# Kernel optimization log

Measured on AMD Instinct MI355X. Metric: run time of the kernel, lower is better.

Reference implementation:

```python
import jax, jax.numpy as jnp
import numpy as np

BN_EPS = 1e-5


def conv1x1(x, w, b):
    # x: [B,C,H,W], w: [O,C], b: [O]
    return jnp.einsum('bchw,oc->bohw', x, w) + b[None, :, None, None]


def dwconv3(x, w, b):
    # depthwise 3x3, SAME padding; w: [C,1,3,3]
    y = jax.lax.conv_general_dilated(
        x, w, window_strides=(1, 1), padding='SAME',
        feature_group_count=x.shape[1],
        dimension_numbers=('NCHW', 'OIHW', 'NCHW'))
    return y + b[None, :, None, None]


def setup_inputs() -> dict:
    key = jax.random.key(0)
    B, C, H, W, E = 8, 256, 80, 80, 2
    ks = jax.random.split(key, 16)

    def n(k, shape, sc=0.02):
        return jax.random.normal(k, shape, dtype=jnp.float32) * sc

    return {
        'x': jax.random.normal(ks[0], (B, C, H, W), dtype=jnp.float32),
        # BatchNorm2d (inference: running stats + affine)
        'bn_gamma': jnp.ones((C,), jnp.float32),
        'bn_beta': jnp.zeros((C,), jnp.float32),
        'bn_mean': n(ks[1], (C,), 0.1),
        'bn_var': jnp.abs(n(ks[2], (C,), 0.5)) + 1.0,
        # SpectralGating complex per-channel gate
        'alpha_real': n(ks[3], (1, C, 1, 1), 0.1),
        'alpha_imag': n(ks[4], (1, C, 1, 1), 0.1),
        # LocalMamba2D (fallback path)
        'pi_w': n(ks[5], (C, C)), 'pi_b': jnp.zeros((C,), jnp.float32),
        'dw_w': n(ks[6], (C, 1, 3, 3)), 'dw_b': jnp.zeros((C,), jnp.float32),
        'fpw_w': n(ks[7], (C, C)), 'fpw_b': jnp.zeros((C,), jnp.float32),
        'ffn1_w': n(ks[8], (C * E, C)), 'ffn1_b': jnp.zeros((C * E,), jnp.float32),
        'ffn2_w': n(ks[9], (C, C * E)), 'ffn2_b': jnp.zeros((C,), jnp.float32),
        'po_w': n(ks[10], (C, C)), 'po_b': jnp.zeros((C,), jnp.float32),
        # post 1x1 conv
        'post_w': n(ks[11], (C, C)), 'post_b': jnp.zeros((C,), jnp.float32),
    }


def reference(x, bn_gamma, bn_beta, bn_mean, bn_var, alpha_real, alpha_imag,
              pi_w, pi_b, dw_w, dw_b, fpw_w, fpw_b,
              ffn1_w, ffn1_b, ffn2_w, ffn2_b, po_w, po_b,
              post_w, post_b):
    res = x
    # pre_norm: BatchNorm2d in inference mode
    inv = jax.lax.rsqrt(bn_var + BN_EPS)
    h = (x - bn_mean[None, :, None, None]) * (bn_gamma * inv)[None, :, None, None] \
        + bn_beta[None, :, None, None]
    # SpectralGating: rfft2 (ortho) -> complex per-channel gate -> irfft2
    H, W = h.shape[2], h.shape[3]
    X = jnp.fft.rfft2(h, norm='ortho')              # [B,C,H,W//2+1] complex
    Y = X * (alpha_real + 1j * alpha_imag)
    h = jnp.fft.irfft2(Y, s=(H, W), norm='ortho')
    # LocalMamba2D fallback: proj_in -> dw3x3 -> GELU -> 1x1 -> FFN -> proj_out (+res)
    # H,W are multiples of window=8, so pad branch is a no-op.
    res2 = h
    t = conv1x1(h, pi_w, pi_b)
    y = jax.nn.gelu(dwconv3(t, dw_w, dw_b), approximate=False)
    y = conv1x1(y, fpw_w, fpw_b)
    y = jax.nn.gelu(conv1x1(y, ffn1_w, ffn1_b), approximate=False)
    y = conv1x1(y, ffn2_w, ffn2_b)
    h = conv1x1(y, po_w, po_b) + res2
    # post 1x1 conv + outer residual
    out = conv1x1(h, post_w, post_b)
    return out + res
```

## Files before the change

### kernel.cpp

```cpp
#include <hip/hip_runtime.h>
#include <cmath>

#define BB 8
#define CC 256
#define HH 80
#define WW 80
#define HWSZ 6400
#define PLANE_FLOATS (CC * HWSZ)
#define TENSOR_FLOATS (BB * PLANE_FLOATS)

using short8v = __attribute__((ext_vector_type(8))) short;
using f32x4  = __attribute__((ext_vector_type(4))) float;

__device__ __forceinline__ float gelu_exact(float v) {
    return 0.5f * v * (1.0f + erff(v * 0.70710678118654752440f));
}

__device__ __forceinline__ unsigned short f2bf(float f) {
    unsigned int u = __float_as_uint(f);
    unsigned int r = (u + 0x7FFFu + ((u >> 16) & 1u)) >> 16;
    return (unsigned short)r;
}
__device__ __forceinline__ float bf2f(unsigned short h) {
    return __uint_as_float(((unsigned int)h) << 16);
}

__global__ __launch_bounds__(256)
void combine_po_post(const float* __restrict__ po_w, const float* __restrict__ po_b,
                     const float* __restrict__ post_w, const float* __restrict__ post_b,
                     float* __restrict__ Wcomb, float* __restrict__ bcomb)
{
    __shared__ float red[256];
    const int o = blockIdx.x;
    const int c = threadIdx.x;
    const float* prow = post_w + (size_t)o * 256;
    float s = 0.f;
#pragma unroll 4
    for (int m = 0; m < 256; ++m)
        s = fmaf(prow[m], po_w[(size_t)m * 256 + c], s);
    Wcomb[(size_t)o * 512 + c] = s;
    Wcomb[(size_t)o * 512 + 256 + c] = prow[c];
    red[c] = prow[c] * po_b[c];
    __syncthreads();
    for (int st = 128; st > 0; st >>= 1) {
        if (c < st) red[c] += red[c + st];
        __syncthreads();
    }
    if (c == 0) bcomb[o] = red[0] + post_b[o];
}

struct PreAll {
    const float* src[7];
    int stride[7];
    int runs[7];
    int dstOff[7];
};

__global__ __launch_bounds__(256)
void preconvert_kernel(PreAll d, unsigned short* __restrict__ packH,
                       unsigned short* __restrict__ packL)
{
    const int m = blockIdx.y;
    const int r = blockIdx.x * 256 + threadIdx.x;
    if (r >= d.runs[m]) return;
    const int ks = r >> 10;
    const int rem = r & 1023;
    const int fi = rem >> 6;
    const int l = rem & 63;
    const int o = fi * 16 + (l & 15);
    const int c0 = ks * 32 + ((l >> 4)) * 8;
    const float* src = d.src[m] + (size_t)o * d.stride[m] + c0;
    short8v hv, lv;
#pragma unroll
    for (int j = 0; j < 8; ++j) {
        const float v = src[j];
        const unsigned short h = f2bf(v);
        const unsigned short lo = f2bf(v - bf2f(h));
        hv[j] = (short)h; lv[j] = (short)lo;
    }
    *(short8v*)(packH + d.dstOff[m] + (size_t)r * 8) = hv;
    *(short8v*)(packL + d.dstOff[m] + (size_t)r * 8) = lv;
}

struct GTab { float g[40]; };

__global__ __launch_bounds__(256)
void bn_gate_kernel(const float* __restrict__ x,
                    const float* __restrict__ gamma, const float* __restrict__ beta,
                    const float* __restrict__ mean,  const float* __restrict__ var,
                    const float* __restrict__ ar,    const float* __restrict__ ai,
                    float* __restrict__ out, GTab gt)
{
    __shared__ float sv[HWSZ];
    const int blk = blockIdx.x;
    const int c = blk & (CC - 1);
    const float sc = gamma[c] * rsqrtf(var[c] + 1e-5f);
    const float sh = beta[c] - mean[c] * sc;
    const float a = ar[c], bgate = ai[c];
    const size_t base = (size_t)blk * HWSZ;

    const float4* x4 = (const float4*)(x + base);
    float4* s4 = (float4*)sv;
    for (int i = threadIdx.x; i < HWSZ / 4; i += 256) {
        float4 v = x4[i];
        v.x = fmaf(sc, v.x, sh); v.y = fmaf(sc, v.y, sh);
        v.z = fmaf(sc, v.z, sh); v.w = fmaf(sc, v.w, sh);
        s4[i] = v;
    }
    __syncthreads();

#pragma unroll 1
    for (int r = 0; r < 4; ++r) {
        const int gi = r * 256 + threadIdx.x;
        if (gi >= 800) break;
        const int y = gi / 10;
        const int x0 = (gi - y * 10) * 8;
        const float* row = sv + y * WW;

        float rbuf[88];
#pragma unroll
        for (int q = 0; q < 22; ++q) {
            int col = x0 + 4 * q;
            if (col >= 80) col -= 80;
            const float4 v = *(const float4*)&row[col];
            rbuf[4 * q + 0] = v.x; rbuf[4 * q + 1] = v.y;
            rbuf[4 * q + 2] = v.z; rbuf[4 * q + 3] = v.w;
        }
        float outv[8];
#pragma unroll
        for (int e = 0; e < 8; ++e) {
            float acc = 0.0f;
#pragma unroll
            for (int jj = 0; jj < 40; ++jj) {
                const int j = 2 * jj + 1;
                acc = fmaf(gt.g[jj], rbuf[80 + e - j], acc);
            }
            outv[e] = fmaf(a, rbuf[80 + e], bgate * acc);
        }
        float4 o0 = {outv[0], outv[1], outv[2], outv[3]};
        float4 o1 = {outv[4], outv[5], outv[6], outv[7]};
        *(float4*)&out[base + (size_t)y * WW + x0]     = o0;
        *(float4*)&out[base + (size_t)y * WW + x0 + 4] = o1;
    }
}

template <int EPI, int KS>
__global__ __launch_bounds__(256)
void gemm_mfma(const float* __restrict__ X, const float* __restrict__ X2,
               const unsigned short* __restrict__ Wh,
               const unsigned short* __restrict__ Wl,
               const float* __restrict__ bias,
               const float* __restrict__ res, float* __restrict__ Y)
{
    __shared__ short8v sB[2][2][256];

    const int bz = blockIdx.z;
    const int nBase = blockIdx.x * 64;
    const int t = threadIdx.x;
    const int l = t & 63;
    const int w = t >> 6;

    const float* Xb  = X + (size_t)bz * PLANE_FLOATS + nBase;
    const float* X2b = (KS == 16) ? (X2 + (size_t)bz * PLANE_FLOATS + nBase) : nullptr;
    float* Yb = Y + (size_t)bz * PLANE_FLOATS;

    const int sn = t & 63;
    const int scg = t >> 6;
    const int slot = ((sn >> 4) * 64) + scg * 16 + (sn & 15);

    f32x4 acc[4][4];
#pragma unroll
    for (int m = 0; m < 4; ++m)
#pragma unroll
        for (int n2 = 0; n2 < 4; ++n2) acc[m][n2] = (f32x4){0.f, 0.f, 0.f, 0.f};

    short8v ah[4], al[4];
    {
        const size_t fb = ((size_t)(w * 4) * 64 + l) * 8;
#pragma unroll
        for (int m = 0; m < 4; ++m) {
            ah[m] = *(const short8v*)(Wh + fb + (size_t)m * 512);
            al[m] = *(const short8v*)(Wl + fb + (size_t)m * 512);
        }
    }
    float xbuf[3][8];
#pragma unroll
    for (int d = 0; d < 3; ++d) {
        if (d < KS) {
            const float* src = (KS == 16 && d >= 8) ? X2b : Xb;
            const int kk = (KS == 16 && d >= 8) ? d - 8 : d;
#pragma unroll
            for (int j = 0; j < 8; ++j)
                xbuf[d][j] = src[(size_t)(kk * 32 + scg * 8 + j) * HWSZ + sn];
        }
    }
    {
        short8v hv, lv;
#pragma unroll
        for (int j = 0; j < 8; ++j) {
            const unsigned short h = f2bf(xbuf[0][j]);
            const unsigned short lo = f2bf(xbuf[0][j] - bf2f(h));
            hv[j] = (short)h; lv[j] = (short)lo;
        }
        sB[0][0][slot] = hv; sB[0][1][slot] = lv;
    }
    __syncthreads();

#pragma unroll
    for (int ks = 0; ks < KS; ++ks) {
        const int p = ks & 1;
        short8v bh[4], bl[4];
#pragma unroll
        for (int n2 = 0; n2 < 4; ++n2) {
            bh[n2] = sB[p][0][n2 * 64 + l];
            bl[n2] = sB[p][1][n2 * 64 + l];
        }
        short8v ah2[4], al2[4];
        if (ks + 1 < KS) {
            const size_t fb = ((size_t)((ks + 1) * 16 + w * 4) * 64 + l) * 8;
#pragma unroll
            for (int m = 0; m < 4; ++m) {
                ah2[m] = *(const short8v*)(Wh + fb + (size_t)m * 512);
                al2[m] = *(const short8v*)(Wl + fb + (size_t)m * 512);
            }
        }
        if (ks + 3 < KS) {
            const int kn = ks + 3;
            const float* src = (KS == 16 && kn >= 8) ? X2b : Xb;
            const int kk = (KS == 16 && kn >= 8) ? kn - 8 : kn;
#pragma unroll
            for (int j = 0; j < 8; ++j)
                xbuf[ks % 3][j] = src[(size_t)(kk * 32 + scg * 8 + j) * HWSZ + sn];
        }
#pragma unroll
        for (int m = 0; m < 4; ++m)
#pragma unroll
            for (int n2 = 0; n2 < 4; ++n2) {
                acc[m][n2] = __builtin_amdgcn_mfma_f32_16x16x32_bf16(
                    ah[m], bh[n2], acc[m][n2], 0, 0, 0);
                acc[m][n2] = __builtin_amdgcn_mfma_f32_16x16x32_bf16(
                    ah[m], bl[n2], acc[m][n2], 0, 0, 0);
                acc[m][n2] = __builtin_amdgcn_mfma_f32_16x16x32_bf16(
                    al[m], bh[n2], acc[m][n2], 0, 0, 0);
            }
        if (ks + 1 < KS) {
            short8v hv, lv;
#pragma unroll
            for (int j = 0; j < 8; ++j) {
                const float v = xbuf[(ks + 1) % 3][j];
                const unsigned short h = f2bf(v);
                const unsigned short lo = f2bf(v - bf2f(h));
                hv[j] = (short)h; lv[j] = (short)lo;
            }
            sB[p ^ 1][0][slot] = hv; sB[p ^ 1][1][slot] = lv;
            __syncthreads();
#pragma unroll
            for (int m = 0; m < 4; ++m) { ah[m] = ah2[m]; al[m] = al2[m]; }
        }
    }

    const int col = l & 15, g = l >> 4;
#pragma unroll
    for (int m = 0; m < 4; ++m) {
        const int o0 = w * 64 + m * 16 + g * 4;
#pragma unroll
        for (int r = 0; r < 4; ++r) {
            const int o = o0 + r;
            const float bo = bias[o];
            float* yrow = Yb + (size_t)o * HWSZ + nBase;
            const float* rrow = (EPI == 2)
                ? (res + ((size_t)bz * CC + o) * HWSZ + nBase) : nullptr;
#pragma unroll
            for (int n2 = 0; n2 < 4; ++n2) {
                const int n = n2 * 16 + col;
                float v = acc[m][n2][r] + bo;
                if (EPI == 1) v = gelu_exact(v);
                if (EPI == 2) v += rrow[n];
                yrow[n] = v;
            }
        }
    }
}

__global__ __launch_bounds__(256)
void dwconv_gelu_kernel(const float* __restrict__ in, const float* __restrict__ w,
                        const float* __restrict__ bias, float* __restrict__ out)
{
    const int g = blockIdx.x * 256 + threadIdx.x;
    const int plane = g / 1600;
    const int pg = g - plane * 1600;
    const int c = plane & (CC - 1);
    const int y = pg / 20;
    const int x0 = (pg - y * 20) * 4;
    const float* p = in + (size_t)plane * HWSZ;

    float rb[3][12];
#pragma unroll
    for (int ky = 0; ky < 3; ++ky) {
        const int yy = y + ky - 1;
        const bool yok = (yy >= 0) && (yy < HH);
        const float* prow = p + yy * WW;
#pragma unroll
        for (int q = 0; q < 3; ++q) {
            const int cx = x0 + 4 * q - 4;
            float4 v = {0.f, 0.f, 0.f, 0.f};
            if (yok && cx >= 0 && cx < WW) v = *(const float4*)&prow[cx];
            rb[ky][4 * q + 0] = v.x; rb[ky][4 * q + 1] = v.y;
            rb[ky][4 * q + 2] = v.z; rb[ky][4 * q + 3] = v.w;
        }
    }
    const float* wc = w + c * 9;
    float wv[9];
#pragma unroll
    for (int k = 0; k < 9; ++k) wv[k] = wc[k];
    const float bo = bias[c];

    float4 res;
    float* rp = (float*)&res;
#pragma unroll
    for (int e = 0; e < 4; ++e) {
        float s = bo;
#pragma unroll
        for (int ky = 0; ky < 3; ++ky)
#pragma unroll
            for (int kx = 0; kx < 3; ++kx)
                s = fmaf(wv[ky * 3 + kx], rb[ky][e + kx + 3], s);
        rp[e] = gelu_exact(s);
    }
    *(float4*)&out[(size_t)plane * HWSZ + (size_t)y * WW + x0] = res;
}

extern "C" void kernel_launch(void* const* d_in, const int* in_sizes, int n_in,
                              void* d_out, int out_size, void* d_ws, size_t ws_size,
                              hipStream_t stream)
{
    const float* x        = (const float*)d_in[0];
    const float* bn_gamma = (const float*)d_in[1];
    const float* bn_beta  = (const float*)d_in[2];
    const float* bn_mean  = (const float*)d_in[3];
    const float* bn_var   = (const float*)d_in[4];
    const float* alpha_r  = (const float*)d_in[5];
    const float* alpha_i  = (const float*)d_in[6];
    const float* pi_w     = (const float*)d_in[7];
    const float* pi_b     = (const float*)d_in[8];
    const float* dw_w     = (const float*)d_in[9];
    const float* dw_b     = (const float*)d_in[10];
    const float* fpw_w    = (const float*)d_in[11];
    const float* fpw_b    = (const float*)d_in[12];
    const float* ffn1_w   = (const float*)d_in[13];
    const float* ffn1_b   = (const float*)d_in[14];
    const float* ffn2_w   = (const float*)d_in[15];
    const float* ffn2_b   = (const float*)d_in[16];
    const float* po_w     = (const float*)d_in[17];
    const float* po_b     = (const float*)d_in[18];
    const float* post_w   = (const float*)d_in[19];
    const float* post_b   = (const float*)d_in[20];

    float* bufA = (float*)d_ws;
    float* bufB = bufA + TENSOR_FLOATS;
    float* bufC = bufB + TENSOR_FLOATS;
    float* bufD = (float*)d_out;
    unsigned short* packH = (unsigned short*)(bufC + TENSOR_FLOATS);
    unsigned short* packL = packH + 524288;
    float* Wcomb = (float*)(packL + 524288);
    float* bcomb = Wcomb + 131072;

    GTab gt;
    for (int jj = 0; jj < 40; ++jj) {
        const int j = 2 * jj + 1;
        double s = 0.0;
        for (int k = 1; k <= 39; ++k)
            s += sin(2.0 * 3.14159265358979323846 * (double)k * (double)j / 80.0);
        gt.g[jj] = (float)(-s / 40.0);
    }

    PreAll pd;
    pd.src[0] = pi_w;              pd.stride[0] = 256; pd.runs[0] = 8192;  pd.dstOff[0] = 0;
    pd.src[1] = fpw_w;             pd.stride[1] = 256; pd.runs[1] = 8192;  pd.dstOff[1] = 65536;
    pd.src[2] = ffn1_w;            pd.stride[2] = 256; pd.runs[2] = 8192;  pd.dstOff[2] = 131072;
    pd.src[3] = ffn1_w + 256*256;  pd.stride[3] = 256; pd.runs[3] = 8192;  pd.dstOff[3] = 196608;
    pd.src[4] = ffn2_w;            pd.stride[4] = 512; pd.runs[4] = 16384; pd.dstOff[4] = 262144;
    pd.src[5] = Wcomb;             pd.stride[5] = 512; pd.runs[5] = 16384; pd.dstOff[5] = 393216;
    pd.src[6] = pi_w;              pd.stride[6] = 256; pd.runs[6] = 0;     pd.dstOff[6] = 0;

    const dim3 gGrid(HWSZ / 64, 1, BB);
    const dim3 gBlk(256);

    combine_po_post<<<256, 256, 0, stream>>>(po_w, po_b, post_w, post_b, Wcomb, bcomb);
    preconvert_kernel<<<dim3(64, 6), 256, 0, stream>>>(pd, packH, packL);
    bn_gate_kernel<<<BB * CC, 256, 0, stream>>>(x, bn_gamma, bn_beta, bn_mean,
                                                bn_var, alpha_r, alpha_i, bufA, gt);
    gemm_mfma<0, 8><<<gGrid, gBlk, 0, stream>>>(bufA, nullptr, packH, packL,
                                                pi_b, nullptr, bufB);
    dwconv_gelu_kernel<<<TENSOR_FLOATS / 1024, 256, 0, stream>>>(bufB, dw_w, dw_b, bufC);
    gemm_mfma<0, 8><<<gGrid, gBlk, 0, stream>>>(bufC, nullptr, packH + 65536,
                                                packL + 65536, fpw_b, nullptr, bufB);
    gemm_mfma<1, 8><<<gGrid, gBlk, 0, stream>>>(bufB, nullptr, packH + 131072,
                                                packL + 131072, ffn1_b, nullptr, bufC);
    gemm_mfma<1, 8><<<gGrid, gBlk, 0, stream>>>(bufB, nullptr, packH + 196608,
                                                packL + 196608, ffn1_b + 256, nullptr, bufD);
    gemm_mfma<0, 16><<<gGrid, gBlk, 0, stream>>>(bufC, bufD, packH + 262144,
                                                 packL + 262144, ffn2_b, nullptr, bufB);
    gemm_mfma<2, 16><<<gGrid, gBlk, 0, stream>>>(bufB, bufA, packH + 393216,
                                                 packL + 393216, bcomb, x, (float*)d_out);
}
```

Measured before the change: 468.8 us.

## Load GEMM activations straight into MFMA registers, drop LDS staging, halve pixel tile

The MFMA GEMM no longer stages activations through shared memory with barriers. Each wave loads its B-fragment directly from global memory in MFMA layout and double-buffers it in registers. The pixel tile shrinks from 64 to 32 columns, doubling the grid. Each wave now repeats the activation load and the bf16 split that were previously shared across the block, and the bf16 high part is truncated instead of rounded. The aim is to remove LDS traffic and __syncthreads stalls and raise occupancy, at the cost of more redundant global loads and less weight reuse per block.

```diff
diff --git a/kernel.cpp b/kernel.cpp
--- a/kernel.cpp
+++ b/kernel.cpp
@@ -152,90 +152,69 @@
                const float* __restrict__ bias,
                const float* __restrict__ res, float* __restrict__ Y)
 {
-    __shared__ short8v sB[2][2][256];
-
     const int bz = blockIdx.z;
-    const int nBase = blockIdx.x * 64;
+    const int nBase = blockIdx.x * 32;
     const int t = threadIdx.x;
     const int l = t & 63;
     const int w = t >> 6;
-
-    const float* Xb  = X + (size_t)bz * PLANE_FLOATS + nBase;
-    const float* X2b = (KS == 16) ? (X2 + (size_t)bz * PLANE_FLOATS + nBase) : nullptr;
+    const int g = l >> 4, col = l & 15;
+
+    const float* Xb = X + (size_t)bz * PLANE_FLOATS + (size_t)g * 8 * HWSZ + nBase + col;
+    const float* X2b = (KS == 16)
+        ? (X2 + (size_t)bz * PLANE_FLOATS + (size_t)g * 8 * HWSZ + nBase + col) : nullptr;
     float* Yb = Y + (size_t)bz * PLANE_FLOATS;
 
-    const int sn = t & 63;
-    const int scg = t >> 6;
-    const int slot = ((sn >> 4) * 64) + scg * 16 + (sn & 15);
-
-    f32x4 acc[4][4];
+    f32x4 acc[4][2];
 #pragma unroll
     for (int m = 0; m < 4; ++m)
 #pragma unroll
-        for (int n2 = 0; n2 < 4; ++n2) acc[m][n2] = (f32x4){0.f, 0.f, 0.f, 0.f};
+        for (int n2 = 0; n2 < 2; ++n2) acc[m][n2] = (f32x4){0.f, 0.f, 0.f, 0.f};
+
+    float xv[2][2][8];
+#pragma unroll
+    for (int n2 = 0; n2 < 2; ++n2)
+#pragma unroll
+        for (int j = 0; j < 8; ++j)
+            xv[0][n2][j] = Xb[(size_t)j * HWSZ + n2 * 16];
 
     short8v ah[4], al[4];
-    {
-        const size_t fb = ((size_t)(w * 4) * 64 + l) * 8;
-#pragma unroll
-        for (int m = 0; m < 4; ++m) {
-            ah[m] = *(const short8v*)(Wh + fb + (size_t)m * 512);
-            al[m] = *(const short8v*)(Wl + fb + (size_t)m * 512);
-        }
-    }
-    float xbuf[3][8];
-#pragma unroll
-    for (int d = 0; d < 3; ++d) {
-        if (d < KS) {
-            const float* src = (KS == 16 && d >= 8) ? X2b : Xb;
-            const int kk = (KS == 16 && d >= 8) ? d - 8 : d;
-#pragma unroll
-            for (int j = 0; j < 8; ++j)
-                xbuf[d][j] = src[(size_t)(kk * 32 + scg * 8 + j) * HWSZ + sn];
-        }
-    }
-    {
-        short8v hv, lv;
-#pragma unroll
-        for (int j = 0; j < 8; ++j) {
-            const unsigned short h = f2bf(xbuf[0][j]);
-            const unsigned short lo = f2bf(xbuf[0][j] - bf2f(h));
-            hv[j] = (short)h; lv[j] = (short)lo;
-        }
-        sB[0][0][slot] = hv; sB[0][1][slot] = lv;
-    }
-    __syncthreads();
 
 #pragma unroll
     for (int ks = 0; ks < KS; ++ks) {
-        const int p = ks & 1;
-        short8v bh[4], bl[4];
-#pragma unroll
-        for (int n2 = 0; n2 < 4; ++n2) {
-            bh[n2] = sB[p][0][n2 * 64 + l];
-            bl[n2] = sB[p][1][n2 * 64 + l];
-        }
-        short8v ah2[4], al2[4];
+        const int cur = ks & 1;
+        {
+            const size_t fb = ((size_t)(ks * 16 + w * 4) * 64 + l) * 8;
+#pragma unroll
+            for (int m = 0; m < 4; ++m) {
+                ah[m] = *(const short8v*)(Wh + fb + (size_t)m * 512);
+                al[m] = *(const short8v*)(Wl + fb + (size_t)m * 512);
+            }
+        }
         if (ks + 1 < KS) {
-            const size_t fb = ((size_t)((ks + 1) * 16 + w * 4) * 64 + l) * 8;
-#pragma unroll
-            for (int m = 0; m < 4; ++m) {
-                ah2[m] = *(const short8v*)(Wh + fb + (size_t)m * 512);
-                al2[m] = *(const short8v*)(Wl + fb + (size_t)m * 512);
-            }
-        }
-        if (ks + 3 < KS) {
-            const int kn = ks + 3;
+            const int kn = ks + 1;
             const float* src = (KS == 16 && kn >= 8) ? X2b : Xb;
             const int kk = (KS == 16 && kn >= 8) ? kn - 8 : kn;
 #pragma unroll
-            for (int j = 0; j < 8; ++j)
-                xbuf[ks % 3][j] = src[(size_t)(kk * 32 + scg * 8 + j) * HWSZ + sn];
-        }
+            for (int n2 = 0; n2 < 2; ++n2)
+#pragma unroll
+                for (int j = 0; j < 8; ++j)
+                    xv[cur ^ 1][n2][j] = src[((size_t)kk * 32 + j) * HWSZ + n2 * 16];
+        }
+        short8v bh[2], bl[2];
+#pragma unroll
+        for (int n2 = 0; n2 < 2; ++n2)
+#pragma unroll
+            for (int j = 0; j < 8; ++j) {
+                const float v = xv[cur][n2][j];
+                const unsigned int u = __float_as_uint(v);
+                bh[n2][j] = (short)(u >> 16);
+                const float lof = v - __uint_as_float(u & 0xFFFF0000u);
+                bl[n2][j] = (short)(__float_as_uint(lof) >> 16);
+            }
 #pragma unroll
         for (int m = 0; m < 4; ++m)
 #pragma unroll
-            for (int n2 = 0; n2 < 4; ++n2) {
+            for (int n2 = 0; n2 < 2; ++n2) {
                 acc[m][n2] = __builtin_amdgcn_mfma_f32_16x16x32_bf16(
                     ah[m], bh[n2], acc[m][n2], 0, 0, 0);
                 acc[m][n2] = __builtin_amdgcn_mfma_f32_16x16x32_bf16(
@@ -243,23 +222,8 @@
                 acc[m][n2] = __builtin_amdgcn_mfma_f32_16x16x32_bf16(
                     al[m], bh[n2], acc[m][n2], 0, 0, 0);
             }
-        if (ks + 1 < KS) {
-            short8v hv, lv;
-#pragma unroll
-            for (int j = 0; j < 8; ++j) {
-                const float v = xbuf[(ks + 1) % 3][j];
-                const unsigned short h = f2bf(v);
-                const unsigned short lo = f2bf(v - bf2f(h));
-                hv[j] = (short)h; lv[j] = (short)lo;
-            }
-            sB[p ^ 1][0][slot] = hv; sB[p ^ 1][1][slot] = lv;
-            __syncthreads();
-#pragma unroll
-            for (int m = 0; m < 4; ++m) { ah[m] = ah2[m]; al[m] = al2[m]; }
-        }
-    }
-
-    const int col = l & 15, g = l >> 4;
+    }
+
 #pragma unroll
     for (int m = 0; m < 4; ++m) {
         const int o0 = w * 64 + m * 16 + g * 4;
@@ -271,7 +235,7 @@
             const float* rrow = (EPI == 2)
                 ? (res + ((size_t)bz * CC + o) * HWSZ + nBase) : nullptr;
 #pragma unroll
-            for (int n2 = 0; n2 < 4; ++n2) {
+            for (int n2 = 0; n2 < 2; ++n2) {
                 const int n = n2 * 16 + col;
                 float v = acc[m][n2][r] + bo;
                 if (EPI == 1) v = gelu_exact(v);
@@ -383,7 +347,7 @@
     pd.src[5] = Wcomb;             pd.stride[5] = 512; pd.runs[5] = 16384; pd.dstOff[5] = 393216;
     pd.src[6] = pi_w;              pd.stride[6] = 256; pd.runs[6] = 0;     pd.dstOff[6] = 0;
 
-    const dim3 gGrid(HWSZ / 64, 1, BB);
+    const dim3 gGrid(HWSZ / 32, 1, BB);
     const dim3 gBlk(256);
 
     combine_po_post<<<256, 256, 0, stream>>>(po_w, po_b, post_w, post_b, Wcomb, bcomb);
```

Result: slower. 507.4 us (+8.2%).
